# Kernel tuning notes

Hardware: AMD Instinct MI355X
Metric: run time of the kernel (lower is better)

The kernel has to match this reference:

```python
import jax, jax.numpy as jnp
import numpy as np

B, N, C, D = 4, 8192, 256, 256
WS = [2048, 4096, 8192]
RS = [1, 2, 4]
HEAD_IDX = 0


def setup_inputs() -> dict:
    key = jax.random.key(0)
    k1, k2, k3, k4 = jax.random.split(key, 4)
    scale = 1.0 / np.sqrt(C).astype(np.float32)
    x = jax.random.normal(k1, (B, N, C), jnp.float32)
    Wq = jax.random.normal(k2, (C, D), jnp.float32) * scale
    Wk = jax.random.normal(k3, (C, D), jnp.float32) * scale
    Wv = jax.random.normal(k4, (C, D), jnp.float32) * scale
    return {"x": x, "Wq": Wq, "Wk": Wk, "Wv": Wv}


def _causal_attn(v, Wq, Wk, Wv):
    # v: [Bseg, m, c] -> out [Bseg, m, D], denom [Bseg, m] (= sum_k exp(score))
    q = v @ Wq
    k = v @ Wk
    val = v @ Wv
    scores = jnp.einsum('bqd,bkd->bqk', q, k) / jnp.sqrt(jnp.asarray(D, v.dtype))
    m = v.shape[1]
    mask = jnp.tril(jnp.ones((m, m), bool))
    scores = jnp.where(mask, scores, -jnp.inf)
    mx = scores.max(-1)  # diagonal always unmasked -> finite
    e = jnp.exp(scores - mx[..., None])
    ssum = e.sum(-1)
    out = jnp.einsum('bqk,bkd->bqd', e, val) / ssum[..., None]
    denom = ssum * jnp.exp(mx)  # unnormalized softmax denominator
    return out, denom


def _dilated_forward(x, Wq, Wk, Wv):
    b, n, c = x.shape
    segs, idx_list = [], []
    for w, r in zip(WS, RS):
        off = HEAD_IDX % r
        s_cnt = n // w
        # [b, s, m, c] strided gather (offset::r within each window of size w)
        xr = x.reshape(b, s_cnt, w, c)[:, :, off::r, :]
        # segment-major then batch, matching torch.cat(..., dim=0) order
        segs.append(jnp.transpose(xr, (1, 0, 2, 3)).reshape(s_cnt * b, -1, c))
        pos = jnp.arange(off, w, r)
        idx_list.append(jnp.arange(s_cnt)[:, None] * w + pos[None, :])  # [s, m]
    batched = jnp.concatenate(segs, 0)  # [28, 2048, c]
    o_b, den_b = _causal_attn(batched, Wq, Wk, Wv)

    # per-token denominator sums across overlapping segments (scatter-add)
    sums = jnp.zeros((b, n), x.dtype)
    per_cfg = []
    start = 0
    for (w, r), idx in zip(zip(WS, RS), idx_list):
        s_cnt = n // w
        cnt = s_cnt * b
        o = jnp.transpose(o_b[start:start + cnt].reshape(s_cnt, b, -1, D), (1, 0, 2, 3))
        d = jnp.transpose(den_b[start:start + cnt].reshape(s_cnt, b, -1), (1, 0, 2))
        start += cnt
        flat_idx = idx.reshape(-1)  # [s*m]
        o_f = o.reshape(b, -1, D)
        d_f = d.reshape(b, -1)
        per_cfg.append((o_f, d_f, flat_idx))
        sums = sums.at[:, flat_idx].add(d_f)

    # weighted scatter-add of outputs, alpha = denom / denom_sum
    out = jnp.zeros((b, n, D), x.dtype)
    for o_f, d_f, flat_idx in per_cfg:
        alphas = d_f / sums[:, flat_idx]
        out = out.at[:, flat_idx, :].add(o_f * alphas[..., None])
    return out


def reference(x, Wq, Wk, Wv):
    return _dilated_forward(x, Wq, Wk, Wv)
```

## Files before the change

### kernel.cpp

```cpp
#include <hip/hip_runtime.h>
#include <hip/hip_bf16.h>

typedef __bf16 bf16;
typedef unsigned short u16;
typedef bf16 bf16x8 __attribute__((ext_vector_type(8)));
typedef bf16 bf16x2 __attribute__((ext_vector_type(2)));
typedef u16  u16x8  __attribute__((ext_vector_type(8)));
typedef u16  u16x4  __attribute__((ext_vector_type(4)));
typedef float f32x4 __attribute__((ext_vector_type(4)));

#define MFMA16(a,b,c) __builtin_amdgcn_mfma_f32_16x16x32_bf16((a),(b),(c),0,0,0)
#define QSCALE 0.09016844005625f

__device__ inline unsigned pack2(float a, float b) {
    bf16x2 t; t[0] = (bf16)a; t[1] = (bf16)b;
    return __builtin_bit_cast(unsigned, t);
}

__global__ void cvt_w(const float* __restrict__ Wq, const float* __restrict__ Wk,
                      const float* __restrict__ Wv, bf16* __restrict__ Wbt) {
    int idx = blockIdx.x * 256 + threadIdx.x;
    int which = idx >> 16;
    int rem = idx & 65535;
    int c = rem >> 8, d = rem & 255;
    const float* W = (which == 0) ? Wq : (which == 1) ? Wk : Wv;
    Wbt[(size_t)which * 65536 + d * 256 + c] = (bf16)W[c * 256 + d];
}

__global__ __launch_bounds__(256, 2)
void qkv_gemm(const float* __restrict__ x, const bf16* __restrict__ Wbt,
              bf16* __restrict__ Qb, bf16* __restrict__ Kb,
              bf16* __restrict__ Vtt1, bf16* __restrict__ Vtt2, bf16* __restrict__ Vtt4) {
    __shared__ __align__(16) u16 lA[64 * 136];
    __shared__ __align__(16) u16 lB[64 * 136];
    int mt = blockIdx.x, which = blockIdx.y;
    int tid = threadIdx.x, wv = tid >> 6, lane = tid & 63;
    int l15 = lane & 15, quad = lane >> 4;

    f32x4 acc[4][4] = {};
    const float* Ax = x + (size_t)(mt * 64) * 256;
    const bf16* Bw = Wbt + (size_t)which * 65536;
    int row = tid >> 2, c0 = (tid & 3) * 32;

    for (int kh = 0; kh < 2; kh++) {
        __syncthreads();
        #pragma unroll
        for (int i = 0; i < 4; i++) {
            float4 f0 = *(const float4*)(Ax + row * 256 + kh * 128 + c0 + i * 8);
            float4 f1 = *(const float4*)(Ax + row * 256 + kh * 128 + c0 + i * 8 + 4);
            bf16x8 v;
            v[0] = (bf16)f0.x; v[1] = (bf16)f0.y; v[2] = (bf16)f0.z; v[3] = (bf16)f0.w;
            v[4] = (bf16)f1.x; v[5] = (bf16)f1.y; v[6] = (bf16)f1.z; v[7] = (bf16)f1.w;
            *(bf16x8*)((bf16*)lA + row * 136 + c0 + i * 8) = v;
        }
        for (int nt = 0; nt < 4; nt++) {
            __syncthreads();
            #pragma unroll
            for (int i = 0; i < 4; i++)
                *(bf16x8*)((bf16*)lB + row * 136 + c0 + i * 8) =
                    *(const bf16x8*)(Bw + (size_t)(nt * 64 + row) * 256 + kh * 128 + c0 + i * 8);
            __syncthreads();
            #pragma unroll
            for (int ks = 0; ks < 4; ks++) {
                bf16x8 a = *(const bf16x8*)((bf16*)lA + (wv * 16 + l15) * 136 + ks * 32 + quad * 8);
                #pragma unroll
                for (int ns = 0; ns < 4; ns++) {
                    bf16x8 b2 = *(const bf16x8*)((bf16*)lB + (ns * 16 + l15) * 136 + ks * 32 + quad * 8);
                    acc[nt][ns] = MFMA16(a, b2, acc[nt][ns]);
                }
            }
        }
    }

    u16* lT = lA;
    float sc = (which == 0) ? QSCALE : 1.0f;
    for (int nt = 0; nt < 4; nt++) {
        __syncthreads();
        if (which < 2) {
            #pragma unroll
            for (int ns = 0; ns < 4; ns++)
                #pragma unroll
                for (int r = 0; r < 4; r++) {
                    bf16 v = (bf16)(acc[nt][ns][r] * sc);
                    lT[(wv * 16 + quad * 4 + r) * 72 + ns * 16 + l15] = *(u16*)&v;
                }
            __syncthreads();
            bf16* outp = (which == 0) ? Qb : Kb;
            int tokl = tid >> 2, ch = tid & 3;
            u16x8 v0 = *(u16x8*)(lT + tokl * 72 + ch * 16);
            u16x8 v1 = *(u16x8*)(lT + tokl * 72 + ch * 16 + 8);
            u16* dst = (u16*)outp + (size_t)(mt * 64 + tokl) * 256 + nt * 64 + ch * 16;
            *(u16x8*)dst = v0;
            *(u16x8*)(dst + 8) = v1;
        } else {
            #pragma unroll
            for (int ns = 0; ns < 4; ns++)
                #pragma unroll
                for (int r = 0; r < 4; r++) {
                    bf16 v = (bf16)acc[nt][ns][r];
                    lT[(ns * 16 + l15) * 72 + wv * 16 + quad * 4 + r] = *(u16*)&v;
                }
            __syncthreads();
            int gtok = mt * 64;
            int bL = gtok >> 13, n0 = gtok & 8191;
            int d_l = tid >> 2, q = tid & 3;
            int dg = nt * 64 + d_l;
            {
                int s1 = n0 >> 11, j1 = n0 & 2047;
                u16* dst = (u16*)Vtt1 + ((size_t)(bL * 4 + s1) * 64 + (j1 >> 5) + (q >> 1)) * 8192
                           + (size_t)dg * 32 + (q & 1) * 16;
                u16x8 a0 = *(u16x8*)(lT + d_l * 72 + q * 16);
                u16x8 a1 = *(u16x8*)(lT + d_l * 72 + q * 16 + 8);
                *(u16x8*)dst = a0; *(u16x8*)(dst + 8) = a1;
            }
            {
                int s2 = n0 >> 12, j2 = (n0 & 4095) >> 1;
                u16x8 e;
                #pragma unroll
                for (int i = 0; i < 8; i++) e[i] = lT[d_l * 72 + q * 16 + 2 * i];
                u16* dst = (u16*)Vtt2 + ((size_t)(bL * 2 + s2) * 64 + (j2 >> 5)) * 8192
                           + (size_t)dg * 32 + q * 8;
                *(u16x8*)dst = e;
            }
            {
                int j4 = n0 >> 2;
                u16x4 e;
                #pragma unroll
                for (int i = 0; i < 4; i++) e[i] = lT[d_l * 72 + q * 16 + 4 * i];
                u16* dst = (u16*)Vtt4 + ((size_t)bL * 64 + (j4 >> 5)) * 8192
                           + (size_t)dg * 32 + (j4 & 31) + q * 4;
                *(u16x4*)dst = e;
            }
        }
    }
}

__global__ __launch_bounds__(256, 2)
void attn(const bf16* __restrict__ Qb, const bf16* __restrict__ Kb,
          const bf16* __restrict__ Vtt1, const bf16* __restrict__ Vtt2,
          const bf16* __restrict__ Vtt4,
          float* __restrict__ O1, float* __restrict__ O2, float* __restrict__ O4,
          float* __restrict__ D1, float* __restrict__ D2, float* __restrict__ D4) {
    __shared__ __align__(16) u16 K_l[2][32 * 264];
    __shared__ __align__(16) u16 V_l[2][256 * 40];

    const int item = (int)blockIdx.x;
    const int qt = 31 - (item / 28);
    const int seg = item % 28;

    int lr, b, s;
    if (seg < 16)      { lr = 0; s = seg >> 2;        b = seg & 3;        }
    else if (seg < 24) { lr = 1; s = (seg - 16) >> 2; b = (seg - 16) & 3; }
    else               { lr = 2; s = 0;               b = seg - 24;       }
    const int rr = 1 << lr;
    const size_t base = (size_t)b * 8192 + (size_t)s * (2048 << lr);
    const size_t pbase = (size_t)b * (8192 >> lr) + (size_t)s * 2048;
    const int segi = (lr == 0) ? (b * 4 + s) : (lr == 1) ? (b * 2 + s) : b;
    const bf16* Vtt = (lr == 0) ? Vtt1 : (lr == 1) ? Vtt2 : Vtt4;
    const u16* Vseg = (const u16*)Vtt + (size_t)segi * 524288;
    float* Op = (lr == 0) ? O1 : (lr == 1) ? O2 : O4;
    float* Dp = (lr == 0) ? D1 : (lr == 1) ? D2 : D4;

    const int tid = threadIdx.x, wv = tid >> 6, lane = tid & 63;
    const int l15 = lane & 15, quad = lane >> 4;

    const int qi = qt * 64 + wv * 16 + l15;
    const bf16* qp = Qb + (base + (size_t)qi * rr) * 256 + quad * 8;
    bf16x8 qf[8];
    #pragma unroll
    for (int ks = 0; ks < 8; ks++) qf[ks] = *(const bf16x8*)(qp + ks * 32);

    f32x4 o[16] = {};
    float m_run = -1e30f, l_run = 0.f;

    const int krow = tid >> 3, kc = tid & 7;
    const u16* Kp = (const u16*)Kb + base * 256;
    const int vrow = tid >> 2, vcol = (tid & 3) * 8;
    u16x8 kpre[4], vpre[4];

    const int nkt = 2 * (qt + 1);
    {
        const u16* kp = Kp + (size_t)krow * rr * 256;
        #pragma unroll
        for (int i = 0; i < 4; i++) kpre[i] = *(const u16x8*)(kp + (kc + 8 * i) * 8);
        #pragma unroll
        for (int i = 0; i < 4; i++) vpre[i] = *(const u16x8*)(Vseg + (size_t)(tid + 256 * i) * 8);
        #pragma unroll
        for (int i = 0; i < 4; i++)
            *(u16x8*)(K_l[0] + krow * 264 + (kc + 8 * i) * 8) = kpre[i];
        #pragma unroll
        for (int i = 0; i < 4; i++)
            *(u16x8*)(V_l[0] + (vrow + 64 * i) * 40 + vcol) = vpre[i];
        const u16* kp1 = Kp + (size_t)(32 + krow) * rr * 256;
        #pragma unroll
        for (int i = 0; i < 4; i++) kpre[i] = *(const u16x8*)(kp1 + (kc + 8 * i) * 8);
        const u16* vp1 = Vseg + 8192;
        #pragma unroll
        for (int i = 0; i < 4; i++) vpre[i] = *(const u16x8*)(vp1 + (size_t)(tid + 256 * i) * 8);
        __syncthreads();
    }

    for (int kt = 0; kt < nkt; kt++) {
        const int buf = kt & 1;
        if (kt + 1 < nkt) {
            #pragma unroll
            for (int i = 0; i < 4; i++)
                *(u16x8*)(K_l[buf ^ 1] + krow * 264 + (kc + 8 * i) * 8) = kpre[i];
            #pragma unroll
            for (int i = 0; i < 4; i++)
                *(u16x8*)(V_l[buf ^ 1] + (vrow + 64 * i) * 40 + vcol) = vpre[i];
        }
        if (kt + 2 < nkt) {
            const u16* kp = Kp + (size_t)((kt + 2) * 32 + krow) * rr * 256;
            #pragma unroll
            for (int i = 0; i < 4; i++) kpre[i] = *(const u16x8*)(kp + (kc + 8 * i) * 8);
            const u16* vp = Vseg + (size_t)(kt + 2) * 8192;
            #pragma unroll
            for (int i = 0; i < 4; i++) vpre[i] = *(const u16x8*)(vp + (size_t)(tid + 256 * i) * 8);
        }

        f32x4 sf[2] = {};
        #pragma unroll
        for (int ks = 0; ks < 8; ks++) {
            #pragma unroll
            for (int kb = 0; kb < 2; kb++) {
                bf16x8 kf = *(const bf16x8*)((const bf16*)K_l[buf] + (kb * 16 + l15) * 264 + ks * 32 + quad * 8);
                sf[kb] = MFMA16(kf, qf[ks], sf[kb]);
            }
        }
        float mx = -1e30f;
        #pragma unroll
        for (int kb = 0; kb < 2; kb++)
            #pragma unroll
            for (int r = 0; r < 4; r++) {
                float v = sf[kb][r];
                if (kt >= 2 * qt) {
                    int key = kt * 32 + kb * 16 + quad * 4 + r;
                    if (key > qi) v = -1e30f;
                }
                sf[kb][r] = v;
                mx = fmaxf(mx, v);
            }
        mx = fmaxf(mx, __shfl_xor(mx, 16));
        mx = fmaxf(mx, __shfl_xor(mx, 32));
        float mold = m_run;
        float mnew = fmaxf(mold, mx);
        m_run = mnew;
        float a = exp2f(mold - mnew);
        float rs = 0.f;
        #pragma unroll
        for (int kb = 0; kb < 2; kb++)
            #pragma unroll
            for (int r = 0; r < 4; r++) {
                float e = exp2f(sf[kb][r] - mnew);
                sf[kb][r] = e;
                rs += e;
            }
        rs += __shfl_xor(rs, 16);
        rs += __shfl_xor(rs, 32);
        l_run = l_run * a + rs;
        if (__any(mnew > mold)) {
            #pragma unroll
            for (int f = 0; f < 16; f++)
                #pragma unroll
                for (int r = 0; r < 4; r++) o[f][r] *= a;
        }
        unsigned pk00 = pack2(sf[0][0], sf[0][1]);
        unsigned pk01 = pack2(sf[0][2], sf[0][3]);
        unsigned pk10 = pack2(sf[1][0], sf[1][1]);
        unsigned pk11 = pack2(sf[1][2], sf[1][3]);
        int src0 = l15 + 32 * (quad & 1);
        int src1 = src0 + 16;
        unsigned b00 = (unsigned)__shfl((int)pk00, src0, 64);
        unsigned b01 = (unsigned)__shfl((int)pk01, src0, 64);
        unsigned b02 = (unsigned)__shfl((int)pk00, src1, 64);
        unsigned b03 = (unsigned)__shfl((int)pk01, src1, 64);
        unsigned b10 = (unsigned)__shfl((int)pk10, src0, 64);
        unsigned b11 = (unsigned)__shfl((int)pk11, src0, 64);
        unsigned b12 = (unsigned)__shfl((int)pk10, src1, 64);
        unsigned b13 = (unsigned)__shfl((int)pk11, src1, 64);
        bool hi = (quad >> 1) != 0;
        union { bf16x8 v; unsigned u[4]; } pbu;
        pbu.u[0] = hi ? b10 : b00;
        pbu.u[1] = hi ? b11 : b01;
        pbu.u[2] = hi ? b12 : b02;
        pbu.u[3] = hi ? b13 : b03;
        #pragma unroll
        for (int f = 0; f < 16; f++) {
            bf16x8 vf = *(const bf16x8*)((const bf16*)V_l[buf] + (f * 16 + l15) * 40 + quad * 8);
            o[f] = MFMA16(vf, pbu.v, o[f]);
        }
        __syncthreads();
    }

    float invl = 1.0f / l_run;
    size_t pos = pbase + (size_t)qi;
    if (quad == 0) Dp[pos] = l_run * exp2f(m_run);
    float* orow = Op + pos * 256 + quad * 4;
    #pragma unroll
    for (int f = 0; f < 16; f++) {
        f32x4 v;
        #pragma unroll
        for (int r = 0; r < 4; r++) v[r] = o[f][r] * invl;
        *(f32x4*)(orow + f * 16) = v;
    }
}

__global__ void finalize(float* __restrict__ out, const float* __restrict__ O2,
                         const float* __restrict__ O4,
                         const float* __restrict__ D1, const float* __restrict__ D2,
                         const float* __restrict__ D4) {
    int g = blockIdx.x * 256 + threadIdx.x;
    int t = g >> 6, dc = (g & 63) * 4;
    int b = t >> 13, n = t & 8191;
    float d1 = D1[t];
    float4 o1 = *(float4*)(out + (size_t)t * 256 + dc);
    float ax = o1.x * d1, ay = o1.y * d1, az = o1.z * d1, aw = o1.w * d1;
    float den = d1;
    if ((n & 1) == 0) {
        int pos2 = b * 4096 + (n >> 12) * 2048 + ((n & 4095) >> 1);
        float d2 = D2[pos2];
        const float4 o2 = *(const float4*)(O2 + (size_t)pos2 * 256 + dc);
        ax += o2.x * d2; ay += o2.y * d2; az += o2.z * d2; aw += o2.w * d2;
        den += d2;
    }
    if ((n & 3) == 0) {
        int pos4 = b * 2048 + (n >> 2);
        float d4 = D4[pos4];
        const float4 o4 = *(const float4*)(O4 + (size_t)pos4 * 256 + dc);
        ax += o4.x * d4; ay += o4.y * d4; az += o4.z * d4; aw += o4.w * d4;
        den += d4;
    }
    float inv = 1.0f / den;
    float4 r; r.x = ax * inv; r.y = ay * inv; r.z = az * inv; r.w = aw * inv;
    *(float4*)(out + (size_t)t * 256 + dc) = r;
}

extern "C" void kernel_launch(void* const* d_in, const int* in_sizes, int n_in,
                              void* d_out, int out_size, void* d_ws, size_t ws_size,
                              hipStream_t stream) {
    const float* x  = (const float*)d_in[0];
    const float* Wq = (const float*)d_in[1];
    const float* Wk = (const float*)d_in[2];
    const float* Wv = (const float*)d_in[3];
    float* out = (float*)d_out;

    char* ws = (char*)d_ws;
    bf16* Qb   = (bf16*)(ws);
    bf16* Kb   = (bf16*)(ws + 16777216);
    bf16* Vtt1 = (bf16*)(ws + 33554432);
    bf16* Vtt2 = (bf16*)(ws + 50331648);
    bf16* Vtt4 = (bf16*)(ws + 58720256);
    bf16* Wbt  = (bf16*)(ws + 62914560);
    float* O2  = (float*)(ws + 63307776);
    float* O4  = (float*)(ws + 80084992);
    float* D1  = (float*)(ws + 88473600);
    float* D2  = (float*)(ws + 88604672);
    float* D4  = (float*)(ws + 88670208);

    cvt_w<<<768, 256, 0, stream>>>(Wq, Wk, Wv, Wbt);
    qkv_gemm<<<dim3(512, 3), 256, 0, stream>>>(x, Wbt, Qb, Kb, Vtt1, Vtt2, Vtt4);
    attn<<<896, 256, 0, stream>>>(Qb, Kb, Vtt1, Vtt2, Vtt4, out, O2, O4, D1, D2, D4);
    finalize<<<8192, 256, 0, stream>>>(out, O2, O4, D1, D2, D4);
}
```

Measured before the change: 265.8 us.

## Rewrite attention kernel with 32x32 MFMA, persistent atomic scheduling, direct-to-LDS loads

The attention kernel now handles 128 query rows per block using 32x32x16 bf16 MFMA tiles. It runs as a persistent kernel that pulls work items from an atomic counter, which is reset in cvt_w. K and V tiles are copied straight into LDS with global_load_lds and double buffered under explicit waitcnt and barrier control. The online-softmax rescale is deferred until the running max grows by more than a threshold, and MFMA sections get raised wave priority. Together these aim to cut LDS round trips through registers, improve MFMA efficiency and balance the causal workload, at the cost of a changed LDS layout that depends on exact lane mappings being right.

```diff
diff --git a/kernel.cpp b/kernel.cpp
--- a/kernel.cpp
+++ b/kernel.cpp
@@ -8,8 +8,10 @@
 typedef u16  u16x8  __attribute__((ext_vector_type(8)));
 typedef u16  u16x4  __attribute__((ext_vector_type(4)));
 typedef float f32x4 __attribute__((ext_vector_type(4)));
+typedef float f32x16 __attribute__((ext_vector_type(16)));
 
 #define MFMA16(a,b,c) __builtin_amdgcn_mfma_f32_16x16x32_bf16((a),(b),(c),0,0,0)
+#define MFMA32(a,b,c) __builtin_amdgcn_mfma_f32_32x32x16_bf16((a),(b),(c),0,0,0)
 #define QSCALE 0.09016844005625f
 
 __device__ inline unsigned pack2(float a, float b) {
@@ -17,8 +19,16 @@
     return __builtin_bit_cast(unsigned, t);
 }
 
+__device__ __forceinline__ void load_lds16(const void* g, void* l) {
+    __builtin_amdgcn_global_load_lds(
+        (const __attribute__((address_space(1))) unsigned*)g,
+        (__attribute__((address_space(3))) unsigned*)l, 16, 0, 0);
+}
+
 __global__ void cvt_w(const float* __restrict__ Wq, const float* __restrict__ Wk,
-                      const float* __restrict__ Wv, bf16* __restrict__ Wbt) {
+                      const float* __restrict__ Wv, bf16* __restrict__ Wbt,
+                      int* __restrict__ cnt) {
+    if (blockIdx.x == 0 && threadIdx.x == 0) *cnt = 0;
     int idx = blockIdx.x * 256 + threadIdx.x;
     int which = idx >> 16;
     int rem = idx & 65535;
@@ -140,169 +150,170 @@
           const bf16* __restrict__ Vtt1, const bf16* __restrict__ Vtt2,
           const bf16* __restrict__ Vtt4,
           float* __restrict__ O1, float* __restrict__ O2, float* __restrict__ O4,
-          float* __restrict__ D1, float* __restrict__ D2, float* __restrict__ D4) {
-    __shared__ __align__(16) u16 K_l[2][32 * 264];
-    __shared__ __align__(16) u16 V_l[2][256 * 40];
-
-    const int item = (int)blockIdx.x;
-    const int qt = 31 - (item / 28);
-    const int seg = item % 28;
-
-    int lr, b, s;
-    if (seg < 16)      { lr = 0; s = seg >> 2;        b = seg & 3;        }
-    else if (seg < 24) { lr = 1; s = (seg - 16) >> 2; b = (seg - 16) & 3; }
-    else               { lr = 2; s = 0;               b = seg - 24;       }
-    const int rr = 1 << lr;
-    const size_t base = (size_t)b * 8192 + (size_t)s * (2048 << lr);
-    const size_t pbase = (size_t)b * (8192 >> lr) + (size_t)s * 2048;
-    const int segi = (lr == 0) ? (b * 4 + s) : (lr == 1) ? (b * 2 + s) : b;
-    const bf16* Vtt = (lr == 0) ? Vtt1 : (lr == 1) ? Vtt2 : Vtt4;
-    const u16* Vseg = (const u16*)Vtt + (size_t)segi * 524288;
-    float* Op = (lr == 0) ? O1 : (lr == 1) ? O2 : O4;
-    float* Dp = (lr == 0) ? D1 : (lr == 1) ? D2 : D4;
+          float* __restrict__ D1, float* __restrict__ D2, float* __restrict__ D4,
+          int* __restrict__ cnt) {
+    __shared__ __align__(16) char K_l[2][16384];
+    __shared__ __align__(16) char V_l[2][16384];
+    __shared__ int item_s;
 
     const int tid = threadIdx.x, wv = tid >> 6, lane = tid & 63;
-    const int l15 = lane & 15, quad = lane >> 4;
-
-    const int qi = qt * 64 + wv * 16 + l15;
-    const bf16* qp = Qb + (base + (size_t)qi * rr) * 256 + quad * 8;
-    bf16x8 qf[8];
-    #pragma unroll
-    for (int ks = 0; ks < 8; ks++) qf[ks] = *(const bf16x8*)(qp + ks * 32);
-
-    f32x4 o[16] = {};
-    float m_run = -1e30f, l_run = 0.f;
-
-    const int krow = tid >> 3, kc = tid & 7;
-    const u16* Kp = (const u16*)Kb + base * 256;
-    const int vrow = tid >> 2, vcol = (tid & 3) * 8;
-    u16x8 kpre[4], vpre[4];
-
-    const int nkt = 2 * (qt + 1);
-    {
-        const u16* kp = Kp + (size_t)krow * rr * 256;
+    const int l31 = lane & 31, hi = lane >> 5;
+
+    for (;;) {
+        __syncthreads();
+        if (tid == 0) item_s = atomicAdd(cnt, 1);
+        __syncthreads();
+        const int item = item_s;
+        if (item >= 448) break;
+
+        const int qt = 15 - item / 28;
+        const int seg = item % 28;
+        int lr, ss, b;
+        if (seg < 16)      { lr = 0; ss = seg >> 2;        b = seg & 3;        }
+        else if (seg < 24) { lr = 1; ss = (seg - 16) >> 2; b = (seg - 16) & 3; }
+        else               { lr = 2; ss = 0;               b = seg - 24;       }
+        const int rr = 1 << lr;
+        const size_t base = (size_t)b * 8192 + (size_t)ss * (2048 << lr);
+        const size_t pbase = (size_t)b * (8192 >> lr) + (size_t)ss * 2048;
+        const int segi = (lr == 0) ? (b * 4 + ss) : (lr == 1) ? (b * 2 + ss) : b;
+        const u16* Vseg = (const u16*)((lr == 0) ? Vtt1 : (lr == 1) ? Vtt2 : Vtt4)
+                          + (size_t)segi * 524288;
+        float* Op = (lr == 0) ? O1 : (lr == 1) ? O2 : O4;
+        float* Dp = (lr == 0) ? D1 : (lr == 1) ? D2 : D4;
+
+        const int ql = qt * 128 + wv * 32 + l31;
+        const u16* Kp = (const u16*)Kb + base * 256;
+        const int nkt = 4 * (qt + 1);
+
+        bf16x8 qf[16];
+        {
+            const bf16* qp = Qb + (base + (size_t)ql * rr) * 256 + hi * 8;
+            #pragma unroll
+            for (int ks = 0; ks < 16; ks++) qf[ks] = *(const bf16x8*)(qp + ks * 16);
+        }
+
+        auto stage = [&](int t, int bs) {
+            #pragma unroll
+            for (int i = 0; i < 4; i++) {
+                const u16* src = Kp + (size_t)((t * 32 + (tid & 31)) * rr) * 256
+                                 + (i * 8 + (tid >> 5)) * 8;
+                load_lds16(src, &K_l[bs][i * 4096 + wv * 1024]);
+            }
+            #pragma unroll
+            for (int i = 0; i < 4; i++) {
+                const u16* src = Vseg + (size_t)t * 8192 + (size_t)tid * 32 + i * 8;
+                load_lds16(src, &V_l[bs][i * 4096 + wv * 1024]);
+            }
+        };
+
+        f32x16 o[8] = {};
+        float m_run = -1e30f, l_run = 0.f;
+
+        stage(0, 0);
+        stage(1, 1);
+
+        for (int kt = 0; kt < nkt; kt++) {
+            const int buf = kt & 1;
+            if (kt + 1 < nkt) asm volatile("s_waitcnt vmcnt(8)" ::: "memory");
+            else              asm volatile("s_waitcnt vmcnt(0)" ::: "memory");
+            __builtin_amdgcn_s_barrier();
+            __builtin_amdgcn_sched_barrier(0);
+
+            const char* Kbl = K_l[buf];
+            const char* Vbl = V_l[buf];
+
+            f32x16 sv = {};
+            __builtin_amdgcn_s_setprio(1);
+            #pragma unroll
+            for (int ks = 0; ks < 16; ks++) {
+                bf16x8 kf = *(const bf16x8*)(Kbl + ks * 1024 + hi * 512 + l31 * 16);
+                sv = MFMA32(kf, qf[ks], sv);
+            }
+            __builtin_amdgcn_s_setprio(0);
+
+            float mx = -1e30f;
+            const bool diag = (kt >= 4 * qt + wv);
+            #pragma unroll
+            for (int r = 0; r < 16; r++) {
+                float v = sv[r];
+                if (diag) {
+                    int key = kt * 32 + (r & 3) + 8 * (r >> 2) + 4 * hi;
+                    if (key > ql) v = -1e30f;
+                    sv[r] = v;
+                }
+                mx = fmaxf(mx, v);
+            }
+            mx = fmaxf(mx, __shfl_xor(mx, 32));
+
+            if (__any(mx > m_run + 12.0f)) {
+                float mnew = fmaxf(m_run, mx);
+                float fac = exp2f(m_run - mnew);
+                l_run *= fac;
+                #pragma unroll
+                for (int dg = 0; dg < 8; dg++)
+                    #pragma unroll
+                    for (int r = 0; r < 16; r++) o[dg][r] *= fac;
+                m_run = mnew;
+            }
+
+            float rs = 0.f;
+            #pragma unroll
+            for (int r = 0; r < 16; r++) {
+                float e = exp2f(sv[r] - m_run);
+                sv[r] = e;
+                rs += e;
+            }
+            rs += __shfl_xor(rs, 32);
+            l_run += rs;
+
+            unsigned pk[8];
+            #pragma unroll
+            for (int rq = 0; rq < 4; rq++) {
+                pk[2 * rq]     = pack2(sv[4 * rq],     sv[4 * rq + 1]);
+                pk[2 * rq + 1] = pack2(sv[4 * rq + 2], sv[4 * rq + 3]);
+            }
+            #pragma unroll
+            for (int st = 0; st < 2; st++) {
+                unsigned p0 = pk[4 * st],     p1 = pk[4 * st + 1];
+                unsigned p2 = pk[4 * st + 2], p3 = pk[4 * st + 3];
+                unsigned s0 = (unsigned)__shfl_xor((int)p0, 32);
+                unsigned s1 = (unsigned)__shfl_xor((int)p1, 32);
+                unsigned s2 = (unsigned)__shfl_xor((int)p2, 32);
+                unsigned s3 = (unsigned)__shfl_xor((int)p3, 32);
+                union { unsigned u[4]; bf16x8 v; } pb;
+                pb.u[0] = hi ? s2 : p0;
+                pb.u[1] = hi ? s3 : p1;
+                pb.u[2] = hi ? p2 : s0;
+                pb.u[3] = hi ? p3 : s1;
+                __builtin_amdgcn_s_setprio(1);
+                #pragma unroll
+                for (int dg = 0; dg < 8; dg++) {
+                    bf16x8 vf = *(const bf16x8*)(Vbl + (st * 2 + hi) * 4096 + dg * 512 + l31 * 16);
+                    o[dg] = MFMA32(vf, pb.v, o[dg]);
+                }
+                __builtin_amdgcn_s_setprio(0);
+            }
+
+            __builtin_amdgcn_s_barrier();
+            __builtin_amdgcn_sched_barrier(0);
+            if (kt + 2 < nkt) stage(kt + 2, buf);
+        }
+
+        float invl = 1.0f / l_run;
+        size_t pos = pbase + (size_t)ql;
+        if (hi == 0) Dp[pos] = l_run * exp2f(m_run);
+        float* orow = Op + pos * 256 + hi * 4;
         #pragma unroll
-        for (int i = 0; i < 4; i++) kpre[i] = *(const u16x8*)(kp + (kc + 8 * i) * 8);
-        #pragma unroll
-        for (int i = 0; i < 4; i++) vpre[i] = *(const u16x8*)(Vseg + (size_t)(tid + 256 * i) * 8);
-        #pragma unroll
-        for (int i = 0; i < 4; i++)
-            *(u16x8*)(K_l[0] + krow * 264 + (kc + 8 * i) * 8) = kpre[i];
-        #pragma unroll
-        for (int i = 0; i < 4; i++)
-            *(u16x8*)(V_l[0] + (vrow + 64 * i) * 40 + vcol) = vpre[i];
-        const u16* kp1 = Kp + (size_t)(32 + krow) * rr * 256;
-        #pragma unroll
-        for (int i = 0; i < 4; i++) kpre[i] = *(const u16x8*)(kp1 + (kc + 8 * i) * 8);
-        const u16* vp1 = Vseg + 8192;
-        #pragma unroll
-        for (int i = 0; i < 4; i++) vpre[i] = *(const u16x8*)(vp1 + (size_t)(tid + 256 * i) * 8);
-        __syncthreads();
-    }
-
-    for (int kt = 0; kt < nkt; kt++) {
-        const int buf = kt & 1;
-        if (kt + 1 < nkt) {
-            #pragma unroll
-            for (int i = 0; i < 4; i++)
-                *(u16x8*)(K_l[buf ^ 1] + krow * 264 + (kc + 8 * i) * 8) = kpre[i];
-            #pragma unroll
-            for (int i = 0; i < 4; i++)
-                *(u16x8*)(V_l[buf ^ 1] + (vrow + 64 * i) * 40 + vcol) = vpre[i];
-        }
-        if (kt + 2 < nkt) {
-            const u16* kp = Kp + (size_t)((kt + 2) * 32 + krow) * rr * 256;
-            #pragma unroll
-            for (int i = 0; i < 4; i++) kpre[i] = *(const u16x8*)(kp + (kc + 8 * i) * 8);
-            const u16* vp = Vseg + (size_t)(kt + 2) * 8192;
-            #pragma unroll
-            for (int i = 0; i < 4; i++) vpre[i] = *(const u16x8*)(vp + (size_t)(tid + 256 * i) * 8);
-        }
-
-        f32x4 sf[2] = {};
-        #pragma unroll
-        for (int ks = 0; ks < 8; ks++) {
-            #pragma unroll
-            for (int kb = 0; kb < 2; kb++) {
-                bf16x8 kf = *(const bf16x8*)((const bf16*)K_l[buf] + (kb * 16 + l15) * 264 + ks * 32 + quad * 8);
-                sf[kb] = MFMA16(kf, qf[ks], sf[kb]);
-            }
-        }
-        float mx = -1e30f;
-        #pragma unroll
-        for (int kb = 0; kb < 2; kb++)
-            #pragma unroll
-            for (int r = 0; r < 4; r++) {
-                float v = sf[kb][r];
-                if (kt >= 2 * qt) {
-                    int key = kt * 32 + kb * 16 + quad * 4 + r;
-                    if (key > qi) v = -1e30f;
-                }
-                sf[kb][r] = v;
-                mx = fmaxf(mx, v);
-            }
-        mx = fmaxf(mx, __shfl_xor(mx, 16));
-        mx = fmaxf(mx, __shfl_xor(mx, 32));
-        float mold = m_run;
-        float mnew = fmaxf(mold, mx);
-        m_run = mnew;
-        float a = exp2f(mold - mnew);
-        float rs = 0.f;
-        #pragma unroll
-        for (int kb = 0; kb < 2; kb++)
-            #pragma unroll
-            for (int r = 0; r < 4; r++) {
-                float e = exp2f(sf[kb][r] - mnew);
-                sf[kb][r] = e;
-                rs += e;
-            }
-        rs += __shfl_xor(rs, 16);
-        rs += __shfl_xor(rs, 32);
-        l_run = l_run * a + rs;
-        if (__any(mnew > mold)) {
-            #pragma unroll
-            for (int f = 0; f < 16; f++)
-                #pragma unroll
-                for (int r = 0; r < 4; r++) o[f][r] *= a;
-        }
-        unsigned pk00 = pack2(sf[0][0], sf[0][1]);
-        unsigned pk01 = pack2(sf[0][2], sf[0][3]);
-        unsigned pk10 = pack2(sf[1][0], sf[1][1]);
-        unsigned pk11 = pack2(sf[1][2], sf[1][3]);
-        int src0 = l15 + 32 * (quad & 1);
-        int src1 = src0 + 16;
-        unsigned b00 = (unsigned)__shfl((int)pk00, src0, 64);
-        unsigned b01 = (unsigned)__shfl((int)pk01, src0, 64);
-        unsigned b02 = (unsigned)__shfl((int)pk00, src1, 64);
-        unsigned b03 = (unsigned)__shfl((int)pk01, src1, 64);
-        unsigned b10 = (unsigned)__shfl((int)pk10, src0, 64);
-        unsigned b11 = (unsigned)__shfl((int)pk11, src0, 64);
-        unsigned b12 = (unsigned)__shfl((int)pk10, src1, 64);
-        unsigned b13 = (unsigned)__shfl((int)pk11, src1, 64);
-        bool hi = (quad >> 1) != 0;
-        union { bf16x8 v; unsigned u[4]; } pbu;
-        pbu.u[0] = hi ? b10 : b00;
-        pbu.u[1] = hi ? b11 : b01;
-        pbu.u[2] = hi ? b12 : b02;
-        pbu.u[3] = hi ? b13 : b03;
-        #pragma unroll
-        for (int f = 0; f < 16; f++) {
-            bf16x8 vf = *(const bf16x8*)((const bf16*)V_l[buf] + (f * 16 + l15) * 40 + quad * 8);
-            o[f] = MFMA16(vf, pbu.v, o[f]);
-        }
-        __syncthreads();
-    }
-
-    float invl = 1.0f / l_run;
-    size_t pos = pbase + (size_t)qi;
-    if (quad == 0) Dp[pos] = l_run * exp2f(m_run);
-    float* orow = Op + pos * 256 + quad * 4;
-    #pragma unroll
-    for (int f = 0; f < 16; f++) {
-        f32x4 v;
-        #pragma unroll
-        for (int r = 0; r < 4; r++) v[r] = o[f][r] * invl;
-        *(f32x4*)(orow + f * 16) = v;
+        for (int dg = 0; dg < 8; dg++)
+            #pragma unroll
+            for (int rq = 0; rq < 4; rq++) {
+                f32x4 v;
+                v[0] = o[dg][4 * rq]     * invl;
+                v[1] = o[dg][4 * rq + 1] * invl;
+                v[2] = o[dg][4 * rq + 2] * invl;
+                v[3] = o[dg][4 * rq + 3] * invl;
+                *(f32x4*)(orow + dg * 32 + rq * 8) = v;
+            }
     }
 }
 
@@ -357,9 +368,10 @@
     float* D1  = (float*)(ws + 88473600);
     float* D2  = (float*)(ws + 88604672);
     float* D4  = (float*)(ws + 88670208);
-
-    cvt_w<<<768, 256, 0, stream>>>(Wq, Wk, Wv, Wbt);
+    int*   cnt = (int*)(ws + 88702976);
+
+    cvt_w<<<768, 256, 0, stream>>>(Wq, Wk, Wv, Wbt, cnt);
     qkv_gemm<<<dim3(512, 3), 256, 0, stream>>>(x, Wbt, Qb, Kb, Vtt1, Vtt2, Vtt4);
-    attn<<<896, 256, 0, stream>>>(Qb, Kb, Vtt1, Vtt2, Vtt4, out, O2, O4, D1, D2, D4);
+    attn<<<512, 256, 0, stream>>>(Qb, Kb, Vtt1, Vtt2, Vtt4, out, O2, O4, D1, D2, D4, cnt);
     finalize<<<8192, 256, 0, stream>>>(out, O2, O4, D1, D2, D4);
 }
```

Measured after the change: 302.8 us. +13.9%, slower.
